# Kernel optimization log

Measured on AMD Instinct MI355X. Metric: run time of the kernel, lower is better.

The kernel has to match this reference:

```python
import jax, jax.numpy as jnp
import numpy as np
import math

B, C, D_FEAT, D_TASK, HID = 1024, 256, 512, 512, 32


def setup_inputs() -> dict:
    key = jax.random.key(0)
    ks = jax.random.split(key, 10)
    def xavier(k, shape, gain):
        fan_out, fan_in = shape
        a = gain * math.sqrt(6.0 / (fan_in + fan_out))
        return jax.random.uniform(k, shape, jnp.float32, -a, a)
    return {
        "Q": jax.random.normal(ks[0], (B, D_TASK), jnp.float32),
        "features": jax.random.normal(ks[1], (B, C, D_FEAT), jnp.float32),
        "Wk_w": xavier(ks[2], (D_TASK, D_FEAT), 0.1),
        "Wk_b": jnp.zeros((D_TASK,), jnp.float32),
        "Wv_w": xavier(ks[3], (D_TASK, D_FEAT), 0.1),
        "Wv_b": jnp.zeros((D_TASK,), jnp.float32),
        "g1_w": xavier(ks[4], (HID, D_TASK + 1), 1.0),
        "g1_b": jax.random.uniform(ks[5], (HID,), jnp.float32, -1.0, 1.0) / math.sqrt(D_TASK + 1),
        "g2_w": xavier(ks[6], (1, HID), 0.1),
        "g2_b": jnp.zeros((1,), jnp.float32),
    }


def reference(Q, features, Wk_w, Wk_b, Wv_w, Wv_b, g1_w, g1_b, g2_w, g2_b):
    # K, V projections: [B, C, d_task]
    K = jnp.einsum('bcf,tf->bct', features, Wk_w) + Wk_b
    V = jnp.einsum('bcf,tf->bct', features, Wv_w) + Wv_b
    # single-query cross-attention
    scores = jnp.einsum('bt,bct->bc', Q, K) / math.sqrt(D_TASK)  # [B, C]
    weights = jax.nn.softmax(scores, axis=-1)
    feat_read = jnp.einsum('bc,bct->bt', weights, V)  # [B, d_task]
    # gate from (Q, feature scale)
    feat_scale = jnp.mean(jnp.abs(features), axis=(1, 2), keepdims=False)[:, None]  # [B, 1]
    h = jnp.concatenate([Q, feat_scale], axis=-1)  # [B, d_task+1]
    h = jax.nn.gelu(h @ g1_w.T + g1_b, approximate=False)
    gate = jax.nn.sigmoid(h @ g2_w.T + g2_b)  # [B, 1]
    return gate * feat_read, gate
```

## Files before the change

kernel.cpp:

```cpp
#include <hip/hip_runtime.h>
#include <math.h>

constexpr int B = 1024, C = 256, DF = 512, DT = 512, HID = 32;

__global__ __launch_bounds__(256) void qproj_kernel(const float* __restrict__ Q,
                                                    const float* __restrict__ Wk,
                                                    float* __restrict__ qtil) {
    __shared__ __align__(16) float qs[4][DT];
    const int tid = threadIdx.x;
    const int b0 = blockIdx.x * 4;
#pragma unroll
    for (int bb = 0; bb < 4; bb++) {
        qs[bb][tid]       = Q[(b0 + bb) * DT + tid];
        qs[bb][tid + 256] = Q[(b0 + bb) * DT + tid + 256];
    }
    __syncthreads();
    const int f0 = tid * 2;
    float acc0[4] = {0.f, 0.f, 0.f, 0.f};
    float acc1[4] = {0.f, 0.f, 0.f, 0.f};
    for (int t4 = 0; t4 < DT; t4 += 4) {
        float q[4][4];
#pragma unroll
        for (int bb = 0; bb < 4; bb++) {
            float4 qv = *(const float4*)&qs[bb][t4];
            q[bb][0] = qv.x; q[bb][1] = qv.y; q[bb][2] = qv.z; q[bb][3] = qv.w;
        }
#pragma unroll
        for (int k = 0; k < 4; k++) {
            float2 w = *(const float2*)(Wk + (size_t)(t4 + k) * DF + f0);
#pragma unroll
            for (int bb = 0; bb < 4; bb++) {
                acc0[bb] += q[bb][k] * w.x;
                acc1[bb] += q[bb][k] * w.y;
            }
        }
    }
#pragma unroll
    for (int bb = 0; bb < 4; bb++) {
        float2 o; o.x = acc0[bb]; o.y = acc1[bb];
        *(float2*)(qtil + (size_t)(b0 + bb) * DF + f0) = o;
    }
}

__global__ __launch_bounds__(256) void main_kernel(
    const float* __restrict__ Q, const float* __restrict__ feat,
    const float* __restrict__ qtil,
    const float* __restrict__ g1w, const float* __restrict__ g1b,
    const float* __restrict__ g2w, const float* __restrict__ g2b,
    float* __restrict__ rg, float* __restrict__ out1) {

    __shared__ __align__(16) float s_q[DF];
    __shared__ __align__(16) float s_Q[DT];
    __shared__ __align__(16) float s_part[4][DF];
    __shared__ float s_m[4], s_l[4], s_abs[4];
    __shared__ float s_hp[HID][8];
    __shared__ float s_h[HID];

    const int tid  = threadIdx.x;
    const int lane = tid & 63;
    const int wv   = tid >> 6;
    const int b    = blockIdx.x;

    s_q[tid]       = qtil[b * DF + tid];
    s_q[tid + 256] = qtil[b * DF + tid + 256];
    s_Q[tid]       = Q[b * DT + tid];
    s_Q[tid + 256] = Q[b * DT + tid + 256];
    __syncthreads();

    float qreg[8];
    {
        float4 a0 = *(const float4*)&s_q[lane * 8];
        float4 a1 = *(const float4*)&s_q[lane * 8 + 4];
        qreg[0] = a0.x; qreg[1] = a0.y; qreg[2] = a0.z; qreg[3] = a0.w;
        qreg[4] = a1.x; qreg[5] = a1.y; qreg[6] = a1.z; qreg[7] = a1.w;
    }

    const float* fb = feat + (size_t)b * C * DF;
    float r[8] = {0.f, 0.f, 0.f, 0.f, 0.f, 0.f, 0.f, 0.f};
    float m = -INFINITY, l = 0.f, sabs = 0.f;
    const float rs = 0.044194173824159216f;

    for (int c = wv * 64; c < wv * 64 + 64; c += 2) {
        const float* row0 = fb + (size_t)c * DF + lane * 8;
        const float* row1 = row0 + DF;
        float4 x0a = *(const float4*)row0;
        float4 x0b = *(const float4*)(row0 + 4);
        float4 x1a = *(const float4*)row1;
        float4 x1b = *(const float4*)(row1 + 4);
        float v0[8] = {x0a.x, x0a.y, x0a.z, x0a.w, x0b.x, x0b.y, x0b.z, x0b.w};
        float v1[8] = {x1a.x, x1a.y, x1a.z, x1a.w, x1b.x, x1b.y, x1b.z, x1b.w};
        float dot0 = 0.f, dot1 = 0.f;
#pragma unroll
        for (int j = 0; j < 8; j++) {
            dot0 += v0[j] * qreg[j];
            dot1 += v1[j] * qreg[j];
            sabs += fabsf(v0[j]) + fabsf(v1[j]);
        }
#pragma unroll
        for (int off = 1; off < 64; off <<= 1) {
            dot0 += __shfl_xor(dot0, off, 64);
            dot1 += __shfl_xor(dot1, off, 64);
        }
        float s0 = dot0 * rs, s1 = dot1 * rs;
        float m2 = fmaxf(fmaxf(m, s0), s1);
        float a  = __expf(m - m2);
        float p0 = __expf(s0 - m2);
        float p1 = __expf(s1 - m2);
        l = l * a + p0 + p1;
#pragma unroll
        for (int j = 0; j < 8; j++) r[j] = r[j] * a + p0 * v0[j] + p1 * v1[j];
        m = m2;
    }
#pragma unroll
    for (int off = 1; off < 64; off <<= 1) sabs += __shfl_xor(sabs, off, 64);
    if (lane == 0) { s_m[wv] = m; s_l[wv] = l; s_abs[wv] = sabs; }
    __syncthreads();

    float M = fmaxf(fmaxf(s_m[0], s_m[1]), fmaxf(s_m[2], s_m[3]));
    float L = s_l[0] * __expf(s_m[0] - M) + s_l[1] * __expf(s_m[1] - M) +
              s_l[2] * __expf(s_m[2] - M) + s_l[3] * __expf(s_m[3] - M);
    float msc = __expf(m - M);
#pragma unroll
    for (int j = 0; j < 8; j++) s_part[wv][lane * 8 + j] = r[j] * msc;
    float fscale = (s_abs[0] + s_abs[1] + s_abs[2] + s_abs[3]) * (1.0f / (float)(C * DF));
    __syncthreads();

    float invL = 1.0f / L;
#pragma unroll
    for (int k = 0; k < 2; k++) {
        int f = tid + 256 * k;
        float val = (s_part[0][f] + s_part[1][f] + s_part[2][f] + s_part[3][f]) * invL;
        rg[(size_t)b * DF + f] = val;
    }

    {
        int i = tid >> 3, g = tid & 7;
        const float* row = g1w + (size_t)i * (DT + 1);
        float part = 0.f;
        for (int t = g * 64; t < g * 64 + 64; ++t) part += row[t] * s_Q[t];
        if (g == 0) part += row[DT] * fscale;
        s_hp[i][g] = part;
    }
    __syncthreads();
    if (tid < HID) {
        float x = g1b[tid];
#pragma unroll
        for (int g = 0; g < 8; ++g) x += s_hp[tid][g];
        s_h[tid] = 0.5f * x * (1.0f + erff(x * 0.70710678118654752f));
    }
    __syncthreads();
    if (tid == 0) {
        float z = g2b[0];
        for (int i = 0; i < HID; ++i) z += s_h[i] * g2w[i];
        out1[b] = 1.0f / (1.0f + __expf(-z));
    }
}

__global__ __launch_bounds__(512) void vproj_kernel(
    const float* __restrict__ rg, const float* __restrict__ gates,
    const float* __restrict__ Wv, const float* __restrict__ Wvb,
    float* __restrict__ out0) {

    __shared__ __align__(16) float s_r4[4][DF];
    __shared__ __align__(16) float s_o[4][DT];

    const int tid  = threadIdx.x;
    const int lane = tid & 63;
    const int wv   = tid >> 6;
    const int b0   = blockIdx.x * 4;

    {
        const float* src = rg + (size_t)b0 * DF;
        float* dst = &s_r4[0][0];
#pragma unroll
        for (int k = 0; k < 4; k++) dst[tid + 512 * k] = src[tid + 512 * k];
    }
    __syncthreads();

    float rr[4][8];
#pragma unroll
    for (int bb = 0; bb < 4; bb++) {
        float4 a0 = *(const float4*)&s_r4[bb][lane * 8];
        float4 a1 = *(const float4*)&s_r4[bb][lane * 8 + 4];
        rr[bb][0] = a0.x; rr[bb][1] = a0.y; rr[bb][2] = a0.z; rr[bb][3] = a0.w;
        rr[bb][4] = a1.x; rr[bb][5] = a1.y; rr[bb][6] = a1.z; rr[bb][7] = a1.w;
    }
    float g4[4];
#pragma unroll
    for (int bb = 0; bb < 4; bb++) g4[bb] = gates[b0 + bb];

    for (int t = wv * 64; t < wv * 64 + 64; t += 2) {
        const float* w0p = Wv + (size_t)t * DF + lane * 8;
        const float* w1p = w0p + DF;
        float4 w0a = *(const float4*)w0p;
        float4 w0b = *(const float4*)(w0p + 4);
        float4 w1a = *(const float4*)w1p;
        float4 w1b = *(const float4*)(w1p + 4);
        float w0[8] = {w0a.x, w0a.y, w0a.z, w0a.w, w0b.x, w0b.y, w0b.z, w0b.w};
        float w1[8] = {w1a.x, w1a.y, w1a.z, w1a.w, w1b.x, w1b.y, w1b.z, w1b.w};
        float d0[4], d1[4];
#pragma unroll
        for (int bb = 0; bb < 4; bb++) {
            float a = 0.f, c = 0.f;
#pragma unroll
            for (int j = 0; j < 8; j++) {
                a += w0[j] * rr[bb][j];
                c += w1[j] * rr[bb][j];
            }
            d0[bb] = a; d1[bb] = c;
        }
#pragma unroll
        for (int off = 1; off < 64; off <<= 1) {
#pragma unroll
            for (int bb = 0; bb < 4; bb++) {
                d0[bb] += __shfl_xor(d0[bb], off, 64);
                d1[bb] += __shfl_xor(d1[bb], off, 64);
            }
        }
        if (lane == 0) {
            float vb0 = Wvb[t], vb1 = Wvb[t + 1];
#pragma unroll
            for (int bb = 0; bb < 4; bb++) {
                s_o[bb][t]     = g4[bb] * (d0[bb] + vb0);
                s_o[bb][t + 1] = g4[bb] * (d1[bb] + vb1);
            }
        }
    }
    __syncthreads();
    *(float4*)(out0 + (size_t)b0 * DT + 4 * tid) = *(const float4*)(&s_o[0][0] + 4 * tid);
}

extern "C" void kernel_launch(void* const* d_in, const int* in_sizes, int n_in,
                              void* d_out, int out_size, void* d_ws, size_t ws_size,
                              hipStream_t stream) {
    const float* Q    = (const float*)d_in[0];
    const float* feat = (const float*)d_in[1];
    const float* Wk   = (const float*)d_in[2];
    const float* Wv   = (const float*)d_in[4];
    const float* Wvb  = (const float*)d_in[5];
    const float* g1w  = (const float*)d_in[6];
    const float* g1b  = (const float*)d_in[7];
    const float* g2w  = (const float*)d_in[8];
    const float* g2b  = (const float*)d_in[9];
    float* out0 = (float*)d_out;
    float* out1 = out0 + (size_t)B * DT;
    float* qtil = (float*)d_ws;
    float* rg   = (float*)d_ws + (size_t)B * DF;

    hipLaunchKernelGGL(qproj_kernel, dim3(B / 4), dim3(256), 0, stream, Q, Wk, qtil);
    hipLaunchKernelGGL(main_kernel, dim3(B), dim3(256), 0, stream,
                       Q, feat, qtil, g1w, g1b, g2w, g2b, rg, out1);
    hipLaunchKernelGGL(vproj_kernel, dim3(B / 4), dim3(512), 0, stream,
                       rg, out1, Wv, Wvb, out0);
}
```

Before: 790.6 us.

## Fuse query projection, attention and value projection into one kernel

Merges the three kernels into a single 1024-thread kernel where each block processes four batch rows: it projects Q through Wk, streams features for attention with online softmax, computes the gate, and applies Wv. This removes two launches and the workspace round trips for the projected query and the attention readout. In exchange the grid shrinks to 256 large blocks, which limits occupancy and adds serial phases with barriers inside each block.

```diff
diff --git a/kernel.cpp b/kernel.cpp
--- a/kernel.cpp
+++ b/kernel.cpp
@@ -2,85 +2,69 @@
 #include <math.h>
 
 constexpr int B = 1024, C = 256, DF = 512, DT = 512, HID = 32;
-
-__global__ __launch_bounds__(256) void qproj_kernel(const float* __restrict__ Q,
-                                                    const float* __restrict__ Wk,
-                                                    float* __restrict__ qtil) {
-    __shared__ __align__(16) float qs[4][DT];
-    const int tid = threadIdx.x;
-    const int b0 = blockIdx.x * 4;
-#pragma unroll
-    for (int bb = 0; bb < 4; bb++) {
-        qs[bb][tid]       = Q[(b0 + bb) * DT + tid];
-        qs[bb][tid + 256] = Q[(b0 + bb) * DT + tid + 256];
-    }
-    __syncthreads();
-    const int f0 = tid * 2;
-    float acc0[4] = {0.f, 0.f, 0.f, 0.f};
-    float acc1[4] = {0.f, 0.f, 0.f, 0.f};
-    for (int t4 = 0; t4 < DT; t4 += 4) {
-        float q[4][4];
-#pragma unroll
-        for (int bb = 0; bb < 4; bb++) {
-            float4 qv = *(const float4*)&qs[bb][t4];
-            q[bb][0] = qv.x; q[bb][1] = qv.y; q[bb][2] = qv.z; q[bb][3] = qv.w;
-        }
-#pragma unroll
-        for (int k = 0; k < 4; k++) {
-            float2 w = *(const float2*)(Wk + (size_t)(t4 + k) * DF + f0);
-#pragma unroll
-            for (int bb = 0; bb < 4; bb++) {
-                acc0[bb] += q[bb][k] * w.x;
-                acc1[bb] += q[bb][k] * w.y;
-            }
-        }
-    }
-#pragma unroll
-    for (int bb = 0; bb < 4; bb++) {
-        float2 o; o.x = acc0[bb]; o.y = acc1[bb];
-        *(float2*)(qtil + (size_t)(b0 + bb) * DF + f0) = o;
-    }
-}
-
-__global__ __launch_bounds__(256) void main_kernel(
+constexpr int BB = 4;
+
+__global__ __launch_bounds__(1024) void fused_kernel(
     const float* __restrict__ Q, const float* __restrict__ feat,
-    const float* __restrict__ qtil,
+    const float* __restrict__ Wk,
+    const float* __restrict__ Wv, const float* __restrict__ Wvb,
     const float* __restrict__ g1w, const float* __restrict__ g1b,
     const float* __restrict__ g2w, const float* __restrict__ g2b,
-    float* __restrict__ rg, float* __restrict__ out1) {
-
-    __shared__ __align__(16) float s_q[DF];
-    __shared__ __align__(16) float s_Q[DT];
-    __shared__ __align__(16) float s_part[4][DF];
-    __shared__ float s_m[4], s_l[4], s_abs[4];
-    __shared__ float s_hp[HID][8];
-    __shared__ float s_h[HID];
+    float* __restrict__ out0, float* __restrict__ out1) {
+
+    __shared__ __align__(16) float s_Q[BB][DT];
+    __shared__ __align__(16) float s_qt[BB][DF];
+    __shared__ __align__(16) float s_part[16][DF];
+    __shared__ float s_m[16], s_l[16], s_abs[16];
+    __shared__ float s_hp[BB][HID][8];
+    __shared__ float s_h[BB][HID];
+    __shared__ float s_gate[BB];
 
     const int tid  = threadIdx.x;
     const int lane = tid & 63;
     const int wv   = tid >> 6;
-    const int b    = blockIdx.x;
-
-    s_q[tid]       = qtil[b * DF + tid];
-    s_q[tid + 256] = qtil[b * DF + tid + 256];
-    s_Q[tid]       = Q[b * DT + tid];
-    s_Q[tid + 256] = Q[b * DT + tid + 256];
+    const int bb_w = wv >> 2;
+    const int b0   = blockIdx.x * BB;
+
+    {
+        float* dst = &s_Q[0][0];
+        dst[tid]        = Q[(size_t)b0 * DT + tid];
+        dst[tid + 1024] = Q[(size_t)b0 * DT + tid + 1024];
+    }
+    __syncthreads();
+
+    {
+        const int f  = tid & 511;
+        const int bq = tid >> 9;
+        float acc0 = 0.f, acc1 = 0.f;
+        for (int t = 0; t < DT; t += 4) {
+#pragma unroll
+            for (int k = 0; k < 4; k++) {
+                float w = Wk[(size_t)(t + k) * DF + f];
+                acc0 += s_Q[bq][t + k] * w;
+                acc1 += s_Q[bq + 2][t + k] * w;
+            }
+        }
+        s_qt[bq][f]     = acc0;
+        s_qt[bq + 2][f] = acc1;
+    }
     __syncthreads();
 
     float qreg[8];
     {
-        float4 a0 = *(const float4*)&s_q[lane * 8];
-        float4 a1 = *(const float4*)&s_q[lane * 8 + 4];
+        float4 a0 = *(const float4*)&s_qt[bb_w][lane * 8];
+        float4 a1 = *(const float4*)&s_qt[bb_w][lane * 8 + 4];
         qreg[0] = a0.x; qreg[1] = a0.y; qreg[2] = a0.z; qreg[3] = a0.w;
         qreg[4] = a1.x; qreg[5] = a1.y; qreg[6] = a1.z; qreg[7] = a1.w;
     }
 
-    const float* fb = feat + (size_t)b * C * DF;
+    const float* fb = feat + (size_t)(b0 + bb_w) * C * DF;
     float r[8] = {0.f, 0.f, 0.f, 0.f, 0.f, 0.f, 0.f, 0.f};
     float m = -INFINITY, l = 0.f, sabs = 0.f;
     const float rs = 0.044194173824159216f;
 
-    for (int c = wv * 64; c < wv * 64 + 64; c += 2) {
+    const int c0 = (wv & 3) * 64;
+    for (int c = c0; c < c0 + 64; c += 2) {
         const float* row0 = fb + (size_t)c * DF + lane * 8;
         const float* row1 = row0 + DF;
         float4 x0a = *(const float4*)row0;
@@ -116,80 +100,81 @@
     if (lane == 0) { s_m[wv] = m; s_l[wv] = l; s_abs[wv] = sabs; }
     __syncthreads();
 
-    float M = fmaxf(fmaxf(s_m[0], s_m[1]), fmaxf(s_m[2], s_m[3]));
-    float L = s_l[0] * __expf(s_m[0] - M) + s_l[1] * __expf(s_m[1] - M) +
-              s_l[2] * __expf(s_m[2] - M) + s_l[3] * __expf(s_m[3] - M);
-    float msc = __expf(m - M);
-#pragma unroll
-    for (int j = 0; j < 8; j++) s_part[wv][lane * 8 + j] = r[j] * msc;
-    float fscale = (s_abs[0] + s_abs[1] + s_abs[2] + s_abs[3]) * (1.0f / (float)(C * DF));
-    __syncthreads();
-
-    float invL = 1.0f / L;
-#pragma unroll
-    for (int k = 0; k < 2; k++) {
-        int f = tid + 256 * k;
-        float val = (s_part[0][f] + s_part[1][f] + s_part[2][f] + s_part[3][f]) * invL;
-        rg[(size_t)b * DF + f] = val;
-    }
-
-    {
-        int i = tid >> 3, g = tid & 7;
+    {
+        const int w0 = bb_w * 4;
+        float M = fmaxf(fmaxf(s_m[w0], s_m[w0 + 1]), fmaxf(s_m[w0 + 2], s_m[w0 + 3]));
+        float msc = __expf(m - M);
+#pragma unroll
+        for (int j = 0; j < 8; j++) s_part[wv][lane * 8 + j] = r[j] * msc;
+    }
+    __syncthreads();
+
+    float* s_r = &s_qt[0][0];
+    {
+        const int f  = tid & 511;
+        const int bq = tid >> 9;
+#pragma unroll
+        for (int h = 0; h < 2; h++) {
+            const int bb = bq + 2 * h;
+            const int w0 = bb * 4;
+            float M = fmaxf(fmaxf(s_m[w0], s_m[w0 + 1]), fmaxf(s_m[w0 + 2], s_m[w0 + 3]));
+            float L = s_l[w0]     * __expf(s_m[w0]     - M)
+                    + s_l[w0 + 1] * __expf(s_m[w0 + 1] - M)
+                    + s_l[w0 + 2] * __expf(s_m[w0 + 2] - M)
+                    + s_l[w0 + 3] * __expf(s_m[w0 + 3] - M);
+            float val = (s_part[w0][f] + s_part[w0 + 1][f] +
+                         s_part[w0 + 2][f] + s_part[w0 + 3][f]) / L;
+            s_r[bb * DF + f] = val;
+        }
+    }
+
+    {
+        const int bg = tid >> 8;
+        const int i  = (tid >> 3) & 31;
+        const int g  = tid & 7;
         const float* row = g1w + (size_t)i * (DT + 1);
         float part = 0.f;
-        for (int t = g * 64; t < g * 64 + 64; ++t) part += row[t] * s_Q[t];
-        if (g == 0) part += row[DT] * fscale;
-        s_hp[i][g] = part;
-    }
-    __syncthreads();
-    if (tid < HID) {
-        float x = g1b[tid];
-#pragma unroll
-        for (int g = 0; g < 8; ++g) x += s_hp[tid][g];
-        s_h[tid] = 0.5f * x * (1.0f + erff(x * 0.70710678118654752f));
-    }
-    __syncthreads();
-    if (tid == 0) {
+        for (int t = g * 64; t < g * 64 + 64; ++t) part += row[t] * s_Q[bg][t];
+        if (g == 0) {
+            const int w0 = bg * 4;
+            float fscale = (s_abs[w0] + s_abs[w0 + 1] + s_abs[w0 + 2] + s_abs[w0 + 3])
+                           * (1.0f / (float)(C * DF));
+            part += row[DT] * fscale;
+        }
+        s_hp[bg][i][g] = part;
+    }
+    __syncthreads();
+    if (tid < BB * HID) {
+        const int bh = tid >> 5, i = tid & 31;
+        float x = g1b[i];
+#pragma unroll
+        for (int g = 0; g < 8; ++g) x += s_hp[bh][i][g];
+        s_h[bh][i] = 0.5f * x * (1.0f + erff(x * 0.70710678118654752f));
+    }
+    __syncthreads();
+    if (tid < BB) {
         float z = g2b[0];
-        for (int i = 0; i < HID; ++i) z += s_h[i] * g2w[i];
-        out1[b] = 1.0f / (1.0f + __expf(-z));
-    }
-}
-
-__global__ __launch_bounds__(512) void vproj_kernel(
-    const float* __restrict__ rg, const float* __restrict__ gates,
-    const float* __restrict__ Wv, const float* __restrict__ Wvb,
-    float* __restrict__ out0) {
-
-    __shared__ __align__(16) float s_r4[4][DF];
-    __shared__ __align__(16) float s_o[4][DT];
-
-    const int tid  = threadIdx.x;
-    const int lane = tid & 63;
-    const int wv   = tid >> 6;
-    const int b0   = blockIdx.x * 4;
-
-    {
-        const float* src = rg + (size_t)b0 * DF;
-        float* dst = &s_r4[0][0];
-#pragma unroll
-        for (int k = 0; k < 4; k++) dst[tid + 512 * k] = src[tid + 512 * k];
-    }
-    __syncthreads();
-
-    float rr[4][8];
-#pragma unroll
-    for (int bb = 0; bb < 4; bb++) {
-        float4 a0 = *(const float4*)&s_r4[bb][lane * 8];
-        float4 a1 = *(const float4*)&s_r4[bb][lane * 8 + 4];
+        for (int i = 0; i < HID; ++i) z += s_h[tid][i] * g2w[i];
+        float gate = 1.0f / (1.0f + __expf(-z));
+        s_gate[tid] = gate;
+        out1[b0 + tid] = gate;
+    }
+    __syncthreads();
+
+    float* s_o = &s_part[0][0];
+    float rr[BB][8];
+#pragma unroll
+    for (int bb = 0; bb < BB; bb++) {
+        float4 a0 = *(const float4*)&s_r[bb * DF + lane * 8];
+        float4 a1 = *(const float4*)&s_r[bb * DF + lane * 8 + 4];
         rr[bb][0] = a0.x; rr[bb][1] = a0.y; rr[bb][2] = a0.z; rr[bb][3] = a0.w;
         rr[bb][4] = a1.x; rr[bb][5] = a1.y; rr[bb][6] = a1.z; rr[bb][7] = a1.w;
     }
-    float g4[4];
-#pragma unroll
-    for (int bb = 0; bb < 4; bb++) g4[bb] = gates[b0 + bb];
-
-    for (int t = wv * 64; t < wv * 64 + 64; t += 2) {
+    float g4[BB];
+#pragma unroll
+    for (int bb = 0; bb < BB; bb++) g4[bb] = s_gate[bb];
+
+    for (int t = wv * 32; t < wv * 32 + 32; t += 2) {
         const float* w0p = Wv + (size_t)t * DF + lane * 8;
         const float* w1p = w0p + DF;
         float4 w0a = *(const float4*)w0p;
@@ -198,9 +183,9 @@
         float4 w1b = *(const float4*)(w1p + 4);
         float w0[8] = {w0a.x, w0a.y, w0a.z, w0a.w, w0b.x, w0b.y, w0b.z, w0b.w};
         float w1[8] = {w1a.x, w1a.y, w1a.z, w1a.w, w1b.x, w1b.y, w1b.z, w1b.w};
-        float d0[4], d1[4];
-#pragma unroll
-        for (int bb = 0; bb < 4; bb++) {
+        float d0[BB], d1[BB];
+#pragma unroll
+        for (int bb = 0; bb < BB; bb++) {
             float a = 0.f, c = 0.f;
 #pragma unroll
             for (int j = 0; j < 8; j++) {
@@ -212,7 +197,7 @@
 #pragma unroll
         for (int off = 1; off < 64; off <<= 1) {
 #pragma unroll
-            for (int bb = 0; bb < 4; bb++) {
+            for (int bb = 0; bb < BB; bb++) {
                 d0[bb] += __shfl_xor(d0[bb], off, 64);
                 d1[bb] += __shfl_xor(d1[bb], off, 64);
             }
@@ -220,14 +205,17 @@
         if (lane == 0) {
             float vb0 = Wvb[t], vb1 = Wvb[t + 1];
 #pragma unroll
-            for (int bb = 0; bb < 4; bb++) {
-                s_o[bb][t]     = g4[bb] * (d0[bb] + vb0);
-                s_o[bb][t + 1] = g4[bb] * (d1[bb] + vb1);
-            }
-        }
-    }
-    __syncthreads();
-    *(float4*)(out0 + (size_t)b0 * DT + 4 * tid) = *(const float4*)(&s_o[0][0] + 4 * tid);
+            for (int bb = 0; bb < BB; bb++) {
+                s_o[bb * DT + t]     = g4[bb] * (d0[bb] + vb0);
+                s_o[bb * DT + t + 1] = g4[bb] * (d1[bb] + vb1);
+            }
+        }
+    }
+    __syncthreads();
+    {
+        float2 o = ((const float2*)s_o)[tid];
+        *(float2*)(out0 + (size_t)b0 * DT + 2 * tid) = o;
+    }
 }
 
 extern "C" void kernel_launch(void* const* d_in, const int* in_sizes, int n_in,
@@ -244,12 +232,8 @@
     const float* g2b  = (const float*)d_in[9];
     float* out0 = (float*)d_out;
     float* out1 = out0 + (size_t)B * DT;
-    float* qtil = (float*)d_ws;
-    float* rg   = (float*)d_ws + (size_t)B * DF;
-
-    hipLaunchKernelGGL(qproj_kernel, dim3(B / 4), dim3(256), 0, stream, Q, Wk, qtil);
-    hipLaunchKernelGGL(main_kernel, dim3(B), dim3(256), 0, stream,
-                       Q, feat, qtil, g1w, g1b, g2w, g2b, rg, out1);
-    hipLaunchKernelGGL(vproj_kernel, dim3(B / 4), dim3(512), 0, stream,
-                       rg, out1, Wv, Wvb, out0);
+    (void)d_ws; (void)ws_size;
+
+    hipLaunchKernelGGL(fused_kernel, dim3(B / BB), dim3(1024), 0, stream,
+                       Q, feat, Wk, Wv, Wvb, g1w, g1b, g2w, g2b, out0, out1);
 }
```

After: 767.6 us. -2.9%, faster.
